# Kernel optimization log

Hardware: AMD Instinct MI355X
Metric: run time of the kernel (lower is better)

Reference implementation:

```python
import jax, jax.numpy as jnp
import numpy as np


def _avg_conv(x, k):
    # depthwise k x k box filter, same padding (torch F.conv2d groups=C)
    C = x.shape[1]
    w = jnp.ones((C, 1, k, k), x.dtype) / (k * k)
    return jax.lax.conv_general_dilated(
        x, w, window_strides=(1, 1),
        padding=[(k // 2, k // 2), (k // 2, k // 2)],
        feature_group_count=C,
        dimension_numbers=('NCHW', 'OIHW', 'NCHW'))


def _shift_feat(where, features, neig_avg_size):
    # Faithful port of shiftFeat: edge-replicate shift + 1e-4 mask on padded strip,
    # then depthwise box average when neig_avg_size > 1. dilation is overridden to
    # neig_avg_size // 2 when neig_avg_size > 1 (as in the torch code).
    B, C, H, W = features.shape
    d = neig_avg_size // 2 if neig_avg_size > 1 else 1
    dt = features.dtype
    PAD = jnp.asarray(1e-4, dt)
    if where == 'none':
        fs = features
        m = jnp.ones((B, 1, H, W), dt)
    elif where == 'left':
        pad = jnp.broadcast_to(features[:, :, :, -1:], (B, C, H, d))
        fs = jnp.concatenate([features[:, :, :, d:], pad], axis=3)
        m = jnp.concatenate([jnp.ones((B, 1, H, W - d), dt), jnp.full((B, 1, H, d), PAD, dt)], axis=3)
    elif where == 'right':
        pad = jnp.broadcast_to(features[:, :, :, :1], (B, C, H, d))
        fs = jnp.concatenate([pad, features[:, :, :, :-d]], axis=3)
        m = jnp.concatenate([jnp.full((B, 1, H, d), PAD, dt), jnp.ones((B, 1, H, W - d), dt)], axis=3)
    elif where == 'bot':
        pad = jnp.broadcast_to(features[:, :, :1, :], (B, C, d, W))
        fs = jnp.concatenate([pad, features[:, :, :-d, :]], axis=2)
        m = jnp.concatenate([jnp.full((B, 1, d, W), PAD, dt), jnp.ones((B, 1, H - d, W), dt)], axis=2)
    elif where == 'top':
        pad = jnp.broadcast_to(features[:, :, -1:, :], (B, C, d, W))
        fs = jnp.concatenate([features[:, :, d:, :], pad], axis=2)
        m = jnp.concatenate([jnp.ones((B, 1, H - d, W), dt), jnp.full((B, 1, d, W), PAD, dt)], axis=2)
    else:
        raise ValueError('Unknown position')
    if neig_avg_size > 1:
        fs = _avg_conv(fs, neig_avg_size)
    # torch takes mask.mean(dim=1, keepdim=True); mask is constant across channels
    return fs, m


def _cos_sim(f1, m1, f2, m2):
    num = (f1 * f2 * m1 * m2).sum(axis=1, keepdims=True)
    den = (jnp.sqrt(((m1 * f1) ** 2).sum(axis=1, keepdims=True))
           * jnp.sqrt(((m2 * f2) ** 2).sum(axis=1, keepdims=True)))
    return num / den


def _total_sim(features, k):
    f1, m1 = _shift_feat('right', features, k)
    f2, m2 = _shift_feat('left', features, k)
    horiz = _cos_sim(f1, m1, f2, m2)
    f1, m1 = _shift_feat('top', features, k)
    f2, m2 = _shift_feat('bot', features, k)
    verti = _cos_sim(f1, m1, f2, m2)
    return (horiz + verti) / 2  # [B,1,H,W]


def setup_inputs() -> dict:
    key = jax.random.key(0)
    features = jax.random.normal(key, (16, 512, 56, 56), dtype=jnp.float32)
    return {"features": features, "patch_sim_neiref_neisimavgsize": 3}


def reference(features, patch_sim_neiref_neisimavgsize):
    return _total_sim(features, patch_sim_neiref_neisimavgsize)
```

## Files before the change

kernel.cpp:

```cpp
#include <hip/hip_runtime.h>
#include <hip/hip_bf16.h>

#define BB 16
#define CC 512
#define HH 56
#define WW 56
#define HW (HH * WW)
#define NPIX (BB * HW)
#define CGROUPS 8

typedef float v4f __attribute__((ext_vector_type(4)));

__device__ __forceinline__ float dpp_prev(float x) {
    return __int_as_float(__builtin_amdgcn_update_dpp(
        __float_as_int(x), __float_as_int(x), 0x111, 0xf, 0xf, false));
}
__device__ __forceinline__ float dpp_next(float x) {
    return __int_as_float(__builtin_amdgcn_update_dpp(
        __float_as_int(x), __float_as_int(x), 0x101, 0xf, 0xf, false));
}

template <int NITER, bool WRITE_OUT>
__global__ __launch_bounds__(256, 4) void ComputeTotalSim_84267258347855_kernel(
    const float* __restrict__ feat, float* __restrict__ ws, float* __restrict__ out) {
    const int wave = threadIdx.x >> 6;
    const int lane = threadIdx.x & 63;
    const int sc = lane >> 4;
    const int q = lane & 15;
    const int qs = (q <= 13) ? q : 13;
    const int x0 = 4 * qs;
    const int b = blockIdx.z;
    const int cg = blockIdx.x;
    const int y = blockIdx.y * 4 + wave;

    const float mym = (y >= 1) ? 1.f : 0.f;
    const float myp = (y <= HH - 2) ? 1.f : 0.f;
    const float mxm0 = (q == 0) ? 0.f : 1.f;
    const float mxp3 = (q >= 13) ? 0.f : 1.f;

    const int ry0 = (y - 2 < 0) ? 0 : y - 2;
    const int ry1 = (y - 1 < 0) ? 0 : y - 1;
    const int ry3 = (y + 1 > HH - 1) ? HH - 1 : y + 1;
    const int ry4 = (y + 2 > HH - 1) ? HH - 1 : y + 2;

    const float* p = feat + ((size_t)b * CC + (size_t)cg * (4 * NITER) + sc) * HW;
    const float* p0 = p + (ry0 * WW + x0);
    const float* p1 = p + (ry1 * WW + x0);
    const float* p2 = p + (y   * WW + x0);
    const float* p3 = p + (ry3 * WW + x0);
    const float* p4 = p + (ry4 * WW + x0);

    float sA0 = 0, sA1 = 0, sA2 = 0, sA3 = 0;
    float sB0 = 0, sB1 = 0, sB2 = 0, sB3 = 0;
    float sC0 = 0, sC1 = 0, sC2 = 0, sC3 = 0;
    float sD0 = 0, sD1 = 0, sD2 = 0, sD3 = 0;
    float sE0 = 0, sE1 = 0, sE2 = 0, sE3 = 0;
    float sF0 = 0, sF1 = 0, sF2 = 0, sF3 = 0;

#define STEP(A0_, A1_, A2_, A3_, A4_)                                           \
    {                                                                           \
        const float Vx = fmaf(mym, A1_.x, fmaf(myp, A3_.x, A2_.x));             \
        const float Vy = fmaf(mym, A1_.y, fmaf(myp, A3_.y, A2_.y));             \
        const float Vz = fmaf(mym, A1_.z, fmaf(myp, A3_.z, A2_.z));             \
        const float Vw = fmaf(mym, A1_.w, fmaf(myp, A3_.w, A2_.w));             \
        const float t3x = fmaf(mym, A2_.x, fmaf(myp, A4_.x, A3_.x));            \
        const float t3y = fmaf(mym, A2_.y, fmaf(myp, A4_.y, A3_.y));            \
        const float t3z = fmaf(mym, A2_.z, fmaf(myp, A4_.z, A3_.z));            \
        const float t3w = fmaf(mym, A2_.w, fmaf(myp, A4_.w, A3_.w));            \
        const float t4x = fmaf(mym, A0_.x, fmaf(myp, A2_.x, A1_.x));            \
        const float t4y = fmaf(mym, A0_.y, fmaf(myp, A2_.y, A1_.y));            \
        const float t4z = fmaf(mym, A0_.z, fmaf(myp, A2_.z, A1_.z));            \
        const float t4w = fmaf(mym, A0_.w, fmaf(myp, A2_.w, A1_.w));            \
        float Vm2 = dpp_prev(Vz), Vm1 = dpp_prev(Vw);                           \
        float Vp4 = dpp_next(Vx), Vp5 = dpp_next(Vy);                           \
        float w3m = dpp_prev(t3w), w3p = dpp_next(t3x);                         \
        float w4m = dpp_prev(t4w), w4p = dpp_next(t4x);                         \
        if (q == 0) { Vm2 = Vx; Vm1 = Vx; w3m = t3x; w4m = t4x; }               \
        if (q >= 13) { Vp4 = Vw; Vp5 = Vw; w3p = t3w; w4p = t4w; }              \
        const float f10 = fmaf(mxm0, Vm2, Vm1 + Vx);                            \
        const float f11 = Vm1 + Vx + Vy;                                        \
        const float f12 = Vx + Vy + Vz;                                         \
        const float f13 = fmaf(mxp3, Vw, Vy + Vz);                              \
        const float f20 = fmaf(mxm0, Vx, Vy + Vz);                              \
        const float f21 = Vy + Vz + Vw;                                         \
        const float f22 = Vz + Vw + Vp4;                                        \
        const float f23 = fmaf(mxp3, Vp5, Vw + Vp4);                            \
        const float f30 = fmaf(mxm0, w3m, t3x + t3y);                           \
        const float f31 = t3x + t3y + t3z;                                      \
        const float f32 = t3y + t3z + t3w;                                      \
        const float f33 = fmaf(mxp3, w3p, t3z + t3w);                           \
        const float f40 = fmaf(mxm0, w4m, t4x + t4y);                           \
        const float f41 = t4x + t4y + t4z;                                      \
        const float f42 = t4y + t4z + t4w;                                      \
        const float f43 = fmaf(mxp3, w4p, t4z + t4w);                           \
        sA0 = fmaf(f10, f20, sA0); sA1 = fmaf(f11, f21, sA1);                   \
        sA2 = fmaf(f12, f22, sA2); sA3 = fmaf(f13, f23, sA3);                   \
        sB0 = fmaf(f10, f10, sB0); sB1 = fmaf(f11, f11, sB1);                   \
        sB2 = fmaf(f12, f12, sB2); sB3 = fmaf(f13, f13, sB3);                   \
        sC0 = fmaf(f20, f20, sC0); sC1 = fmaf(f21, f21, sC1);                   \
        sC2 = fmaf(f22, f22, sC2); sC3 = fmaf(f23, f23, sC3);                   \
        sD0 = fmaf(f30, f40, sD0); sD1 = fmaf(f31, f41, sD1);                   \
        sD2 = fmaf(f32, f42, sD2); sD3 = fmaf(f33, f43, sD3);                   \
        sE0 = fmaf(f30, f30, sE0); sE1 = fmaf(f31, f31, sE1);                   \
        sE2 = fmaf(f32, f32, sE2); sE3 = fmaf(f33, f33, sE3);                   \
        sF0 = fmaf(f40, f40, sF0); sF1 = fmaf(f41, f41, sF1);                   \
        sF2 = fmaf(f42, f42, sF2); sF3 = fmaf(f43, f43, sF3);                   \
    }

#define LOAD5P(R0, R1, R2, R3, R4)                                              \
    asm volatile("global_load_dwordx4 %0, %1, off" : "=&v"(R0) : "v"(p0));      \
    asm volatile("global_load_dwordx4 %0, %1, off" : "=&v"(R1) : "v"(p1));      \
    asm volatile("global_load_dwordx4 %0, %1, off" : "=&v"(R2) : "v"(p2));      \
    asm volatile("global_load_dwordx4 %0, %1, off" : "=&v"(R3) : "v"(p3));      \
    asm volatile("global_load_dwordx4 %0, %1, off" : "=&v"(R4) : "v"(p4));      \
    p0 += 4 * HW; p1 += 4 * HW; p2 += 4 * HW; p3 += 4 * HW; p4 += 4 * HW;

#define WAITV(N)                                          \
    asm volatile("s_waitcnt vmcnt(" #N ")" ::: "memory"); \
    __builtin_amdgcn_sched_barrier(0);

    v4f A0, A1, A2, A3, A4, B0, B1, B2, B3, B4;

    LOAD5P(A0, A1, A2, A3, A4);
    LOAD5P(B0, B1, B2, B3, B4);
    for (int k = 0; k + 4 <= NITER; k += 2) {
        WAITV(5);
        STEP(A0, A1, A2, A3, A4);
        LOAD5P(A0, A1, A2, A3, A4);
        WAITV(5);
        STEP(B0, B1, B2, B3, B4);
        LOAD5P(B0, B1, B2, B3, B4);
    }
    WAITV(5);
    STEP(A0, A1, A2, A3, A4);
    WAITV(0);
    STEP(B0, B1, B2, B3, B4);
#undef STEP
#undef LOAD5P
#undef WAITV

#define RED2(v) { v += __shfl_xor(v, 16, 64); v += __shfl_xor(v, 32, 64); }
    RED2(sA0) RED2(sA1) RED2(sA2) RED2(sA3)
    RED2(sB0) RED2(sB1) RED2(sB2) RED2(sB3)
    RED2(sC0) RED2(sC1) RED2(sC2) RED2(sC3)
    RED2(sD0) RED2(sD1) RED2(sD2) RED2(sD3)
    RED2(sE0) RED2(sE1) RED2(sE2) RED2(sE3)
    RED2(sF0) RED2(sF1) RED2(sF2) RED2(sF3)
#undef RED2

    if (lane < 14) {
        const int pix = b * HW + y * WW + 4 * q;
        if (WRITE_OUT) {
            v4f r;
            r.x = (float)(0.5 * ((double)sA0 / sqrt((double)sB0 * (double)sC0) +
                                 (double)sD0 / sqrt((double)sE0 * (double)sF0)));
            r.y = (float)(0.5 * ((double)sA1 / sqrt((double)sB1 * (double)sC1) +
                                 (double)sD1 / sqrt((double)sE1 * (double)sF1)));
            r.z = (float)(0.5 * ((double)sA2 / sqrt((double)sB2 * (double)sC2) +
                                 (double)sD2 / sqrt((double)sE2 * (double)sF2)));
            r.w = (float)(0.5 * ((double)sA3 / sqrt((double)sB3 * (double)sC3) +
                                 (double)sD3 / sqrt((double)sE3 * (double)sF3)));
            *(v4f*)(out + pix) = r;
        } else {
            float* slab = ws + (size_t)cg * 6 * NPIX;
            *(v4f*)(slab + 0 * NPIX + pix) = (v4f){sA0, sA1, sA2, sA3};
            *(v4f*)(slab + 1 * NPIX + pix) = (v4f){sB0, sB1, sB2, sB3};
            *(v4f*)(slab + 2 * NPIX + pix) = (v4f){sC0, sC1, sC2, sC3};
            *(v4f*)(slab + 3 * NPIX + pix) = (v4f){sD0, sD1, sD2, sD3};
            *(v4f*)(slab + 4 * NPIX + pix) = (v4f){sE0, sE1, sE2, sE3};
            *(v4f*)(slab + 5 * NPIX + pix) = (v4f){sF0, sF1, sF2, sF3};
        }
    }
}

__global__ void ComputeTotalSim_finalize(const float* __restrict__ ws,
                                         float* __restrict__ out) {
    const int i = blockIdx.x * blockDim.x + threadIdx.x;
    if (i < NPIX / 4) {
        const int px = 4 * i;
        v4f a0 = {0, 0, 0, 0}, a1 = {0, 0, 0, 0}, a2 = {0, 0, 0, 0};
        v4f a3 = {0, 0, 0, 0}, a4 = {0, 0, 0, 0}, a5 = {0, 0, 0, 0};
#pragma unroll
        for (int cg = 0; cg < CGROUPS; ++cg) {
            const float* slab = ws + (size_t)cg * 6 * NPIX;
            a0 += *(const v4f*)(slab + 0 * NPIX + px);
            a1 += *(const v4f*)(slab + 1 * NPIX + px);
            a2 += *(const v4f*)(slab + 2 * NPIX + px);
            a3 += *(const v4f*)(slab + 3 * NPIX + px);
            a4 += *(const v4f*)(slab + 4 * NPIX + px);
            a5 += *(const v4f*)(slab + 5 * NPIX + px);
        }
        v4f r;
        r.x = (float)(0.5 * ((double)a0.x / sqrt((double)a1.x * (double)a2.x) +
                             (double)a3.x / sqrt((double)a4.x * (double)a5.x)));
        r.y = (float)(0.5 * ((double)a0.y / sqrt((double)a1.y * (double)a2.y) +
                             (double)a3.y / sqrt((double)a4.y * (double)a5.y)));
        r.z = (float)(0.5 * ((double)a0.z / sqrt((double)a1.z * (double)a2.z) +
                             (double)a3.z / sqrt((double)a4.z * (double)a5.z)));
        r.w = (float)(0.5 * ((double)a0.w / sqrt((double)a1.w * (double)a2.w) +
                             (double)a3.w / sqrt((double)a4.w * (double)a5.w)));
        *(v4f*)(out + px) = r;
    }
}

extern "C" void kernel_launch(void* const* d_in, const int* in_sizes, int n_in,
                              void* d_out, int out_size, void* d_ws, size_t ws_size,
                              hipStream_t stream) {
    const float* feat = (const float*)d_in[0];
    float* out = (float*)d_out;

    const size_t need = (size_t)CGROUPS * 6 * NPIX * sizeof(float);
    if (ws_size >= need) {
        dim3 grid(CGROUPS, HH / 4, BB);
        ComputeTotalSim_84267258347855_kernel<CC / (4 * CGROUPS), false>
            <<<grid, 256, 0, stream>>>(feat, (float*)d_ws, out);
        ComputeTotalSim_finalize<<<(NPIX / 4 + 255) / 256, 256, 0, stream>>>(
            (const float*)d_ws, out);
    } else {
        dim3 grid(1, HH / 4, BB);
        ComputeTotalSim_84267258347855_kernel<CC / 4, true>
            <<<grid, 256, 0, stream>>>(feat, nullptr, out);
    }
}
```

Measured before the change: 34.06 us.

## Remap lanes to 2 pixels by 2 channels and double channel groups

```diff
diff --git a/kernel.cpp b/kernel.cpp
--- a/kernel.cpp
+++ b/kernel.cpp
@@ -7,28 +7,24 @@
 #define WW 56
 #define HW (HH * WW)
 #define NPIX (BB * HW)
-#define CGROUPS 8
-
+#define CGROUPS 16
+
+typedef float v2f __attribute__((ext_vector_type(2)));
 typedef float v4f __attribute__((ext_vector_type(4)));
 
-__device__ __forceinline__ float dpp_prev(float x) {
-    return __int_as_float(__builtin_amdgcn_update_dpp(
-        __float_as_int(x), __float_as_int(x), 0x111, 0xf, 0xf, false));
-}
-__device__ __forceinline__ float dpp_next(float x) {
-    return __int_as_float(__builtin_amdgcn_update_dpp(
-        __float_as_int(x), __float_as_int(x), 0x101, 0xf, 0xf, false));
+__device__ __forceinline__ float shfl64(float v, int srcLane) {
+    return __shfl(v, srcLane, 64);
 }
 
 template <int NITER, bool WRITE_OUT>
-__global__ __launch_bounds__(256, 4) void ComputeTotalSim_84267258347855_kernel(
+__global__ __launch_bounds__(256, 8) void ComputeTotalSim_84267258347855_kernel(
     const float* __restrict__ feat, float* __restrict__ ws, float* __restrict__ out) {
-    const int wave = threadIdx.x >> 6;
+    const int wave = __builtin_amdgcn_readfirstlane(threadIdx.x >> 6);
     const int lane = threadIdx.x & 63;
-    const int sc = lane >> 4;
-    const int q = lane & 15;
-    const int qs = (q <= 13) ? q : 13;
-    const int x0 = 4 * qs;
+    const int sc = lane >> 5;
+    const int q = lane & 31;
+    const int qs = (q <= 27) ? q : 27;
+    const int x0 = 2 * qs;
     const int b = blockIdx.z;
     const int cg = blockIdx.x;
     const int y = blockIdx.y * 4 + wave;
@@ -36,139 +32,121 @@
     const float mym = (y >= 1) ? 1.f : 0.f;
     const float myp = (y <= HH - 2) ? 1.f : 0.f;
     const float mxm0 = (q == 0) ? 0.f : 1.f;
-    const float mxp3 = (q >= 13) ? 0.f : 1.f;
+    const float mxp1 = (q >= 27) ? 0.f : 1.f;
 
     const int ry0 = (y - 2 < 0) ? 0 : y - 2;
     const int ry1 = (y - 1 < 0) ? 0 : y - 1;
     const int ry3 = (y + 1 > HH - 1) ? HH - 1 : y + 1;
     const int ry4 = (y + 2 > HH - 1) ? HH - 1 : y + 2;
 
-    const float* p = feat + ((size_t)b * CC + (size_t)cg * (4 * NITER) + sc) * HW;
-    const float* p0 = p + (ry0 * WW + x0);
-    const float* p1 = p + (ry1 * WW + x0);
-    const float* p2 = p + (y   * WW + x0);
-    const float* p3 = p + (ry3 * WW + x0);
-    const float* p4 = p + (ry4 * WW + x0);
-
-    float sA0 = 0, sA1 = 0, sA2 = 0, sA3 = 0;
-    float sB0 = 0, sB1 = 0, sB2 = 0, sB3 = 0;
-    float sC0 = 0, sC1 = 0, sC2 = 0, sC3 = 0;
-    float sD0 = 0, sD1 = 0, sD2 = 0, sD3 = 0;
-    float sE0 = 0, sE1 = 0, sE2 = 0, sE3 = 0;
-    float sF0 = 0, sF1 = 0, sF2 = 0, sF3 = 0;
+    const float* p = feat + ((size_t)b * CC + (size_t)cg * (2 * NITER) + sc) * HW;
+
+    float sA0 = 0, sA1 = 0, sB0 = 0, sB1 = 0, sC0 = 0, sC1 = 0;
+    float sD0 = 0, sD1 = 0, sE0 = 0, sE1 = 0, sF0 = 0, sF1 = 0;
 
 #define STEP(A0_, A1_, A2_, A3_, A4_)                                           \
     {                                                                           \
         const float Vx = fmaf(mym, A1_.x, fmaf(myp, A3_.x, A2_.x));             \
         const float Vy = fmaf(mym, A1_.y, fmaf(myp, A3_.y, A2_.y));             \
-        const float Vz = fmaf(mym, A1_.z, fmaf(myp, A3_.z, A2_.z));             \
-        const float Vw = fmaf(mym, A1_.w, fmaf(myp, A3_.w, A2_.w));             \
         const float t3x = fmaf(mym, A2_.x, fmaf(myp, A4_.x, A3_.x));            \
         const float t3y = fmaf(mym, A2_.y, fmaf(myp, A4_.y, A3_.y));            \
-        const float t3z = fmaf(mym, A2_.z, fmaf(myp, A4_.z, A3_.z));            \
-        const float t3w = fmaf(mym, A2_.w, fmaf(myp, A4_.w, A3_.w));            \
         const float t4x = fmaf(mym, A0_.x, fmaf(myp, A2_.x, A1_.x));            \
         const float t4y = fmaf(mym, A0_.y, fmaf(myp, A2_.y, A1_.y));            \
-        const float t4z = fmaf(mym, A0_.z, fmaf(myp, A2_.z, A1_.z));            \
-        const float t4w = fmaf(mym, A0_.w, fmaf(myp, A2_.w, A1_.w));            \
-        float Vm2 = dpp_prev(Vz), Vm1 = dpp_prev(Vw);                           \
-        float Vp4 = dpp_next(Vx), Vp5 = dpp_next(Vy);                           \
-        float w3m = dpp_prev(t3w), w3p = dpp_next(t3x);                         \
-        float w4m = dpp_prev(t4w), w4p = dpp_next(t4x);                         \
+        float Vm2 = shfl64(Vx, lane - 1), Vm1 = shfl64(Vy, lane - 1);           \
+        float Vp0 = shfl64(Vx, lane + 1), Vp1 = shfl64(Vy, lane + 1);           \
+        float w3m = shfl64(t3y, lane - 1), w3p = shfl64(t3x, lane + 1);         \
+        float w4m = shfl64(t4y, lane - 1), w4p = shfl64(t4x, lane + 1);         \
         if (q == 0) { Vm2 = Vx; Vm1 = Vx; w3m = t3x; w4m = t4x; }               \
-        if (q >= 13) { Vp4 = Vw; Vp5 = Vw; w3p = t3w; w4p = t4w; }              \
-        const float f10 = fmaf(mxm0, Vm2, Vm1 + Vx);                            \
-        const float f11 = Vm1 + Vx + Vy;                                        \
-        const float f12 = Vx + Vy + Vz;                                         \
-        const float f13 = fmaf(mxp3, Vw, Vy + Vz);                              \
-        const float f20 = fmaf(mxm0, Vx, Vy + Vz);                              \
-        const float f21 = Vy + Vz + Vw;                                         \
-        const float f22 = Vz + Vw + Vp4;                                        \
-        const float f23 = fmaf(mxp3, Vp5, Vw + Vp4);                            \
-        const float f30 = fmaf(mxm0, w3m, t3x + t3y);                           \
-        const float f31 = t3x + t3y + t3z;                                      \
-        const float f32 = t3y + t3z + t3w;                                      \
-        const float f33 = fmaf(mxp3, w3p, t3z + t3w);                           \
-        const float f40 = fmaf(mxm0, w4m, t4x + t4y);                           \
-        const float f41 = t4x + t4y + t4z;                                      \
-        const float f42 = t4y + t4z + t4w;                                      \
-        const float f43 = fmaf(mxp3, w4p, t4z + t4w);                           \
+        if (q >= 27) { Vp0 = Vy; Vp1 = Vy; w3p = t3y; w4p = t4y; }              \
+        const float u1 = Vm1 + Vx, u2 = Vy + Vp0;                               \
+        const float u3 = t3x + t3y, u4 = t4x + t4y;                             \
+        const float f10 = fmaf(mxm0, Vm2, u1), f11 = fmaf(mxp1, Vy, u1);        \
+        const float f20 = fmaf(mxm0, Vx, u2),  f21 = fmaf(mxp1, Vp1, u2);       \
+        const float f30 = fmaf(mxm0, w3m, u3), f31 = fmaf(mxp1, w3p, u3);       \
+        const float f40 = fmaf(mxm0, w4m, u4), f41 = fmaf(mxp1, w4p, u4);       \
         sA0 = fmaf(f10, f20, sA0); sA1 = fmaf(f11, f21, sA1);                   \
-        sA2 = fmaf(f12, f22, sA2); sA3 = fmaf(f13, f23, sA3);                   \
         sB0 = fmaf(f10, f10, sB0); sB1 = fmaf(f11, f11, sB1);                   \
-        sB2 = fmaf(f12, f12, sB2); sB3 = fmaf(f13, f13, sB3);                   \
         sC0 = fmaf(f20, f20, sC0); sC1 = fmaf(f21, f21, sC1);                   \
-        sC2 = fmaf(f22, f22, sC2); sC3 = fmaf(f23, f23, sC3);                   \
         sD0 = fmaf(f30, f40, sD0); sD1 = fmaf(f31, f41, sD1);                   \
-        sD2 = fmaf(f32, f42, sD2); sD3 = fmaf(f33, f43, sD3);                   \
         sE0 = fmaf(f30, f30, sE0); sE1 = fmaf(f31, f31, sE1);                   \
-        sE2 = fmaf(f32, f32, sE2); sE3 = fmaf(f33, f33, sE3);                   \
         sF0 = fmaf(f40, f40, sF0); sF1 = fmaf(f41, f41, sF1);                   \
-        sF2 = fmaf(f42, f42, sF2); sF3 = fmaf(f43, f43, sF3);                   \
-    }
-
-#define LOAD5P(R0, R1, R2, R3, R4)                                              \
-    asm volatile("global_load_dwordx4 %0, %1, off" : "=&v"(R0) : "v"(p0));      \
-    asm volatile("global_load_dwordx4 %0, %1, off" : "=&v"(R1) : "v"(p1));      \
-    asm volatile("global_load_dwordx4 %0, %1, off" : "=&v"(R2) : "v"(p2));      \
-    asm volatile("global_load_dwordx4 %0, %1, off" : "=&v"(R3) : "v"(p3));      \
-    asm volatile("global_load_dwordx4 %0, %1, off" : "=&v"(R4) : "v"(p4));      \
-    p0 += 4 * HW; p1 += 4 * HW; p2 += 4 * HW; p3 += 4 * HW; p4 += 4 * HW;
+    }
+
+#define LOAD5(R0, R1, R2, R3, R4, PC)                                                      \
+    asm volatile("global_load_dwordx2 %0, %1, off offset:-448" : "=&v"(R0) : "v"(PC));     \
+    asm volatile("global_load_dwordx2 %0, %1, off offset:-224" : "=&v"(R1) : "v"(PC));     \
+    asm volatile("global_load_dwordx2 %0, %1, off"             : "=&v"(R2) : "v"(PC));     \
+    asm volatile("global_load_dwordx2 %0, %1, off offset:224"  : "=&v"(R3) : "v"(PC));     \
+    asm volatile("global_load_dwordx2 %0, %1, off offset:448"  : "=&v"(R4) : "v"(PC));
 
 #define WAITV(N)                                          \
     asm volatile("s_waitcnt vmcnt(" #N ")" ::: "memory"); \
     __builtin_amdgcn_sched_barrier(0);
 
-    v4f A0, A1, A2, A3, A4, B0, B1, B2, B3, B4;
-
-    LOAD5P(A0, A1, A2, A3, A4);
-    LOAD5P(B0, B1, B2, B3, B4);
-    for (int k = 0; k + 4 <= NITER; k += 2) {
+    v2f A0, A1, A2, A3, A4, B0, B1, B2, B3, B4;
+
+    if (blockIdx.y >= 1 && blockIdx.y <= 12) {
+        const float* pc = p + (y * WW + x0);
+        LOAD5(A0, A1, A2, A3, A4, pc); pc += 2 * HW;
+        LOAD5(B0, B1, B2, B3, B4, pc); pc += 2 * HW;
+        for (int k = 0; k + 4 <= NITER; k += 2) {
+            WAITV(5);
+            STEP(A0, A1, A2, A3, A4);
+            LOAD5(A0, A1, A2, A3, A4, pc); pc += 2 * HW;
+            WAITV(5);
+            STEP(B0, B1, B2, B3, B4);
+            LOAD5(B0, B1, B2, B3, B4, pc); pc += 2 * HW;
+        }
         WAITV(5);
         STEP(A0, A1, A2, A3, A4);
-        LOAD5P(A0, A1, A2, A3, A4);
-        WAITV(5);
+        WAITV(0);
         STEP(B0, B1, B2, B3, B4);
-        LOAD5P(B0, B1, B2, B3, B4);
-    }
-    WAITV(5);
-    STEP(A0, A1, A2, A3, A4);
-    WAITV(0);
-    STEP(B0, B1, B2, B3, B4);
+    } else {
+        const int o0 = ry0 * WW + x0, o1 = ry1 * WW + x0, o2 = y * WW + x0,
+                  o3 = ry3 * WW + x0, o4 = ry4 * WW + x0;
+        A0 = *(const v2f*)(p + o0); A1 = *(const v2f*)(p + o1);
+        A2 = *(const v2f*)(p + o2); A3 = *(const v2f*)(p + o3);
+        A4 = *(const v2f*)(p + o4);
+        p += 2 * HW;
+        for (int k = 0; k + 2 <= NITER; k += 2) {
+            B0 = *(const v2f*)(p + o0); B1 = *(const v2f*)(p + o1);
+            B2 = *(const v2f*)(p + o2); B3 = *(const v2f*)(p + o3);
+            B4 = *(const v2f*)(p + o4);
+            STEP(A0, A1, A2, A3, A4);
+            const float* pn = (k + 2 < NITER) ? p + 2 * HW : p;
+            A0 = *(const v2f*)(pn + o0); A1 = *(const v2f*)(pn + o1);
+            A2 = *(const v2f*)(pn + o2); A3 = *(const v2f*)(pn + o3);
+            A4 = *(const v2f*)(pn + o4);
+            STEP(B0, B1, B2, B3, B4);
+            p = pn + 2 * HW;
+        }
+    }
 #undef STEP
-#undef LOAD5P
+#undef LOAD5
 #undef WAITV
 
-#define RED2(v) { v += __shfl_xor(v, 16, 64); v += __shfl_xor(v, 32, 64); }
-    RED2(sA0) RED2(sA1) RED2(sA2) RED2(sA3)
-    RED2(sB0) RED2(sB1) RED2(sB2) RED2(sB3)
-    RED2(sC0) RED2(sC1) RED2(sC2) RED2(sC3)
-    RED2(sD0) RED2(sD1) RED2(sD2) RED2(sD3)
-    RED2(sE0) RED2(sE1) RED2(sE2) RED2(sE3)
-    RED2(sF0) RED2(sF1) RED2(sF2) RED2(sF3)
-#undef RED2
-
-    if (lane < 14) {
-        const int pix = b * HW + y * WW + 4 * q;
+#define RED1(v) { v += __shfl_xor(v, 32, 64); }
+    RED1(sA0) RED1(sA1) RED1(sB0) RED1(sB1) RED1(sC0) RED1(sC1)
+    RED1(sD0) RED1(sD1) RED1(sE0) RED1(sE1) RED1(sF0) RED1(sF1)
+#undef RED1
+
+    if (lane < 28) {
+        const int pix = b * HW + y * WW + 2 * q;
         if (WRITE_OUT) {
-            v4f r;
+            v2f r;
             r.x = (float)(0.5 * ((double)sA0 / sqrt((double)sB0 * (double)sC0) +
                                  (double)sD0 / sqrt((double)sE0 * (double)sF0)));
             r.y = (float)(0.5 * ((double)sA1 / sqrt((double)sB1 * (double)sC1) +
                                  (double)sD1 / sqrt((double)sE1 * (double)sF1)));
-            r.z = (float)(0.5 * ((double)sA2 / sqrt((double)sB2 * (double)sC2) +
-                                 (double)sD2 / sqrt((double)sE2 * (double)sF2)));
-            r.w = (float)(0.5 * ((double)sA3 / sqrt((double)sB3 * (double)sC3) +
-                                 (double)sD3 / sqrt((double)sE3 * (double)sF3)));
-            *(v4f*)(out + pix) = r;
+            *(v2f*)(out + pix) = r;
         } else {
             float* slab = ws + (size_t)cg * 6 * NPIX;
-            *(v4f*)(slab + 0 * NPIX + pix) = (v4f){sA0, sA1, sA2, sA3};
-            *(v4f*)(slab + 1 * NPIX + pix) = (v4f){sB0, sB1, sB2, sB3};
-            *(v4f*)(slab + 2 * NPIX + pix) = (v4f){sC0, sC1, sC2, sC3};
-            *(v4f*)(slab + 3 * NPIX + pix) = (v4f){sD0, sD1, sD2, sD3};
-            *(v4f*)(slab + 4 * NPIX + pix) = (v4f){sE0, sE1, sE2, sE3};
-            *(v4f*)(slab + 5 * NPIX + pix) = (v4f){sF0, sF1, sF2, sF3};
+            *(v2f*)(slab + 0 * NPIX + pix) = (v2f){sA0, sA1};
+            *(v2f*)(slab + 1 * NPIX + pix) = (v2f){sB0, sB1};
+            *(v2f*)(slab + 2 * NPIX + pix) = (v2f){sC0, sC1};
+            *(v2f*)(slab + 3 * NPIX + pix) = (v2f){sD0, sD1};
+            *(v2f*)(slab + 4 * NPIX + pix) = (v2f){sE0, sE1};
+            *(v2f*)(slab + 5 * NPIX + pix) = (v2f){sF0, sF1};
         }
     }
 }
@@ -212,13 +190,13 @@
     const size_t need = (size_t)CGROUPS * 6 * NPIX * sizeof(float);
     if (ws_size >= need) {
         dim3 grid(CGROUPS, HH / 4, BB);
-        ComputeTotalSim_84267258347855_kernel<CC / (4 * CGROUPS), false>
+        ComputeTotalSim_84267258347855_kernel<CC / (2 * CGROUPS), false>
             <<<grid, 256, 0, stream>>>(feat, (float*)d_ws, out);
         ComputeTotalSim_finalize<<<(NPIX / 4 + 255) / 256, 256, 0, stream>>>(
             (const float*)d_ws, out);
     } else {
         dim3 grid(1, HH / 4, BB);
-        ComputeTotalSim_84267258347855_kernel<CC / 4, true>
+        ComputeTotalSim_84267258347855_kernel<CC / 2, true>
             <<<grid, 256, 0, stream>>>(feat, nullptr, out);
     }
 }
```

New measurement: 54.18 us. +59.1%, slower.
